# Kernel optimization log

Measured on AMD Instinct MI355X. Metric: run time of the kernel, lower is better.

Reference implementation:

```python
import jax, jax.numpy as jnp
import numpy as np

B, S, E, CS, NC, H = 4, 2048, 1024, 16, 8, 16
D = E + CS            # d_model = 1040
DH = D // H           # head_dim = 65
DFF = 4 * E           # forward_expansion * embed_size


def setup_inputs() -> dict:
    key = jax.random.key(0)
    ks = jax.random.split(key, 20)
    s = 0.02  # init scale for weights
    f32 = jnp.float32
    return {
        'x': jax.random.normal(ks[0], (B, S, E), f32),
        'conditioning': jax.random.uniform(ks[1], (B, S, CS), f32),
        # attention params (torch Linear convention: W is [out, in])
        'Wq': jax.random.normal(ks[2], (D, D), f32) * s,
        'bq': jnp.zeros((D,), f32),
        'Wv': jax.random.normal(ks[3], (D, D), f32) * s,
        'bv': jnp.zeros((D,), f32),
        'Wk': jax.random.normal(ks[4], (NC, D, D), f32) * s,  # stacked per-class key projections
        'bk': jnp.zeros((NC, D), f32),
        'Wo': jax.random.normal(ks[5], (D, D), f32) * s,
        'bo': jnp.zeros((D,), f32),
        # layernorms
        'g1': jnp.ones((E,), f32), 'bn1': jnp.zeros((E,), f32),
        'g2': jnp.ones((E,), f32), 'bn2': jnp.zeros((E,), f32),
        # feed-forward
        'Wf1': jax.random.normal(ks[6], (DFF, E), f32) * s,
        'bf1': jnp.zeros((DFF,), f32),
        'Wf2': jax.random.normal(ks[7], (E, DFF), f32) * s,
        'bf2': jnp.zeros((E,), f32),
    }


def _layernorm(x, g, b, eps=1e-5):
    m = jnp.mean(x, axis=-1, keepdims=True)
    v = jnp.mean(jnp.square(x - m), axis=-1, keepdims=True)
    return (x - m) * jax.lax.rsqrt(v + eps) * g + b


def reference(x, conditioning, Wq, bq, Wv, bv, Wk, bk, Wo, bo,
              g1, bn1, g2, bn2, Wf1, bf1, Wf2, bf2):
    # dropout is identity (eval mode)
    xn = _layernorm(x, g1, bn1)                       # [B,S,E]
    xc = jnp.concatenate([xn, conditioning], axis=-1)  # [B,S,D]

    q = (xc @ Wq.T + bq).reshape(B, S, H, DH).transpose(0, 2, 1, 3)  # [B,H,S,DH]
    v = (xc @ Wv.T + bv).reshape(B, S, H, DH).transpose(0, 2, 1, 3)

    # per-class keys: [B,C,S,D], then weighted-sum by conditioning[:,:,:NC]
    keys = jnp.einsum('bsd,cod->bcso', xc, Wk) + bk[None, :, None, :]
    w = conditioning[:, :, :NC]                        # [B,S,C]
    k = jnp.einsum('bsc,bcso->bso', w, keys)           # [B,S,D]
    k = k.reshape(B, S, H, DH).transpose(0, 2, 1, 3)   # [B,H,S,DH]

    scale = 1.0 / np.sqrt(DH).astype(np.float32)
    scores = jnp.einsum('bhqd,bhkd->bhqk', q, k) * scale
    attn = jax.nn.softmax(scores, axis=-1)
    o = jnp.einsum('bhqk,bhkd->bhqd', attn, v)
    o = o.transpose(0, 2, 1, 3).reshape(B, S, D)
    o = o @ Wo.T + bo

    h = xn + o[:, :, :E]                               # residual uses normed x
    ff = jnp.maximum(h @ Wf1.T + bf1, 0.0) @ Wf2.T + bf2
    return _layernorm(h + ff, g2, bn2)
```

## Files before the change

kernel.cpp:

```cpp
#include <hip/hip_runtime.h>
#include <hip/hip_bf16.h>
#include <math.h>

typedef __bf16 bf16;
typedef __bf16 v8bf __attribute__((ext_vector_type(8)));
typedef float v4f __attribute__((ext_vector_type(4)));

#define B_   4
#define S_   2048
#define E_   1024
#define CS_  16
#define NC_  8
#define H_   16
#define D_   1040
#define DH_  65
#define DFF_ 4096
#define M_   8192
#define KC_  1056
#define KH_  (4 * KC_)
#define KB2_ (8 * KC_)

__device__ __forceinline__ v4f mfma16(v8bf a, v8bf b, v4f c) {
    return __builtin_amdgcn_mfma_f32_16x16x32_bf16(a, b, c, 0, 0, 0);
}

__device__ __forceinline__ void async16(const bf16* g, bf16* l) {
    __builtin_amdgcn_global_load_lds(
        (const __attribute__((address_space(1))) unsigned int*)g,
        (__attribute__((address_space(3))) unsigned int*)l, 16, 0, 0);
}

__global__ __launch_bounds__(256) void k_cvt(const float* __restrict__ src,
                                             bf16* __restrict__ dst, int n) {
    int i = (blockIdx.x * 256 + threadIdx.x) * 4;
    if (i + 4 <= n) {
        float4 v = *(const float4*)(src + i);
        bf16 o[4] = {(bf16)v.x, (bf16)v.y, (bf16)v.z, (bf16)v.w};
        *(ushort4*)(dst + i) = *(const ushort4*)o;
    }
}

__global__ __launch_bounds__(256) void k_build_bk(const float* __restrict__ Wk,
                                                  bf16* __restrict__ Bp) {
    int c = blockIdx.y;
    int idx = blockIdx.x * 256 + threadIdx.x;
    if (idx >= 1040 * 130) return;
    int n = idx / 130, u = idx - n * 130;
    const float* src = Wk + ((size_t)(c * D_ + n)) * D_ + u * 8;
    float4 a = *(const float4*)src;
    float4 b = *(const float4*)(src + 4);
    bf16 o[8] = {(bf16)a.x, (bf16)a.y, (bf16)a.z, (bf16)a.w,
                 (bf16)b.x, (bf16)b.y, (bf16)b.z, (bf16)b.w};
    *(uint4*)(Bp + (size_t)n * KB2_ + c * KC_ + u * 8) = *(const uint4*)o;
}

__global__ __launch_bounds__(256) void k_scale_a(const bf16* __restrict__ xc,
                                                 const float* __restrict__ cond,
                                                 int coff, bf16* __restrict__ Ap) {
    int idx = blockIdx.x * 256 + threadIdx.x;
    int m = idx / 132, u = idx - m * 132;
    int j = u * 8;
    float4 w4 = *(const float4*)(cond + (size_t)m * CS_ + coff);
    float wv[4] = {w4.x, w4.y, w4.z, w4.w};
    bf16* dst = Ap + (size_t)m * KH_ + j;
    if (j < D_) {
        union { uint4 u4; bf16 h[8]; } src;
        src.u4 = *(const uint4*)(xc + (size_t)m * D_ + j);
        float xv[8];
#pragma unroll
        for (int e = 0; e < 8; ++e) xv[e] = (float)src.h[e];
#pragma unroll
        for (int cc = 0; cc < 4; ++cc) {
            bf16 o[8];
#pragma unroll
            for (int e = 0; e < 8; ++e) o[e] = (bf16)(xv[e] * wv[cc]);
            *(uint4*)(dst + cc * KC_) = *(const uint4*)o;
        }
    } else {
        uint4 z = {0u, 0u, 0u, 0u};
#pragma unroll
        for (int cc = 0; cc < 4; ++cc) *(uint4*)(dst + cc * KC_) = z;
    }
}

__global__ __launch_bounds__(256) void k_zero_pads(bf16* __restrict__ qp,
                                                   bf16* __restrict__ kp) {
    int i = blockIdx.x * 256 + threadIdx.x;
    int row = i >> 3, j = i & 7;
    uint4 z = {0u, 0u, 0u, 0u};
    bf16* base = (j < 4) ? qp : kp;
    ((uint4*)(base + (size_t)row * 96 + 64))[j & 3] = z;
}

__global__ __launch_bounds__(256) void k_ln_concat(
    const float* __restrict__ x, const float* __restrict__ cond,
    const float* __restrict__ g, const float* __restrict__ bn,
    bf16* __restrict__ xc)
{
    int row = blockIdx.x;
    int t = threadIdx.x;
    const float* xr = x + (size_t)row * E_;
    float4 v = *(const float4*)(xr + t * 4);
    float s = v.x + v.y + v.z + v.w;
    float ss = v.x * v.x + v.y * v.y + v.z * v.z + v.w * v.w;
#pragma unroll
    for (int off = 32; off; off >>= 1) {
        s  += __shfl_down(s, off);
        ss += __shfl_down(ss, off);
    }
    __shared__ float red[8];
    int wid = t >> 6;
    if ((t & 63) == 0) { red[wid] = s; red[4 + wid] = ss; }
    __syncthreads();
    float stot  = red[0] + red[1] + red[2] + red[3];
    float sstot = red[4] + red[5] + red[6] + red[7];
    float mean = stot * (1.0f / E_);
    float var  = sstot * (1.0f / E_) - mean * mean;
    float rs = rsqrtf(var + 1e-5f);
    bf16* xcr = xc + (size_t)row * D_;
    float vv[4] = {v.x, v.y, v.z, v.w};
#pragma unroll
    for (int j = 0; j < 4; ++j) {
        int i = t * 4 + j;
        xcr[i] = (bf16)(((vv[j] - mean) * rs) * g[i] + bn[i]);
    }
    if (t < CS_) xcr[E_ + t] = (bf16)cond[(size_t)row * CS_ + t];
}

__global__ __launch_bounds__(256) void k_gemm_k2(
    const bf16* __restrict__ A, const bf16* __restrict__ Bm,
    int koffB, bf16* __restrict__ Pout)
{
    __shared__ bf16 As[128][32];
    __shared__ bf16 Bs[128][32];
    int t = threadIdx.x;

    int pid = blockIdx.x;
    int gid = pid / 72;
    int rem = pid - gid * 72;
    int mi = gid * 8 + (rem & 7);
    int ni = rem >> 3;
    int m0 = mi << 7, n0 = ni << 7;

    int lane = t & 63, w = t >> 6;
    int wm = (w >> 1) * 64, wn = (w & 1) * 64;
    int lr = lane & 15, lq = lane >> 4;

    int row_i[2], seg_i[2];
#pragma unroll
    for (int i = 0; i < 2; ++i) { row_i[i] = (t + i * 256) >> 2; seg_i[i] = (t + i * 256) & 3; }

    v4f acc[4][4];
    v4f vzero = {0.f, 0.f, 0.f, 0.f};
#pragma unroll
    for (int mt = 0; mt < 4; ++mt)
#pragma unroll
        for (int nt = 0; nt < 4; ++nt) acc[mt][nt] = vzero;

    for (int kb = 0; kb < KH_ / 32; ++kb) {
        int k0 = kb << 5;
#pragma unroll
        for (int i = 0; i < 2; ++i) {
            async16(A + (size_t)(m0 + row_i[i]) * KH_ + k0 + seg_i[i] * 8,
                    &As[0][0] + (t + i * 256) * 8);
            async16(Bm + (size_t)(n0 + row_i[i]) * KB2_ + koffB + k0 + seg_i[i] * 8,
                    &Bs[0][0] + (t + i * 256) * 8);
        }
        __syncthreads();
        v8bf af[4], bfr[4];
#pragma unroll
        for (int mt = 0; mt < 4; ++mt) af[mt]  = *(const v8bf*)(&As[wm + mt * 16 + lr][lq * 8]);
#pragma unroll
        for (int nt = 0; nt < 4; ++nt) bfr[nt] = *(const v8bf*)(&Bs[wn + nt * 16 + lr][lq * 8]);
#pragma unroll
        for (int mt = 0; mt < 4; ++mt)
#pragma unroll
            for (int nt = 0; nt < 4; ++nt)
                acc[mt][nt] = mfma16(af[mt], bfr[nt], acc[mt][nt]);
        __syncthreads();
    }

#pragma unroll
    for (int mt = 0; mt < 4; ++mt)
#pragma unroll
        for (int reg = 0; reg < 4; ++reg) {
            int grow = m0 + wm + mt * 16 + lq * 4 + reg;
#pragma unroll
            for (int nt = 0; nt < 4; ++nt) {
                int gcol = n0 + wn + nt * 16 + lr;
                if (gcol < D_)
                    Pout[(size_t)grow * D_ + gcol] = (bf16)acc[mt][nt][reg];
            }
        }
}

__global__ __launch_bounds__(256) void k_comb_k(
    const bf16* __restrict__ P0, const bf16* __restrict__ P1,
    const float* __restrict__ condw, const float* __restrict__ bkp,
    bf16* __restrict__ kp)
{
    int idx = blockIdx.x * 256 + threadIdx.x;
    int m = idx / 1040, n = idx - m * 1040;
    float v = (float)P0[idx] + (float)P1[idx];
#pragma unroll
    for (int c = 0; c < NC_; ++c)
        v += condw[(size_t)m * CS_ + c] * bkp[(size_t)c * D_ + n];
    int h = n / 65, d = n - h * 65;
    int b = m >> 11, s = m & 2047;
    kp[(((size_t)(b * 16 + h)) * S_ + s) * 96 + d] = (bf16)v;
}

#define EP_QV  0
#define EP_O   1
#define EP_FF1 2
#define EP_FF2 3

template<int EP>
__global__ __launch_bounds__(256) void k_gemm(
    const bf16* __restrict__ A, const bf16* __restrict__ Bm,
    const float* __restrict__ bias, const float* __restrict__ bias2,
    int M, int N, int K, int lda, int ldb, int nbn,
    bf16* __restrict__ Cb, float* __restrict__ Cf, int ldc,
    const bf16* __restrict__ res, int ldres, bf16* __restrict__ Cb2)
{
    __shared__ bf16 As[128][32];
    __shared__ bf16 Bs[128][32];
    int t = threadIdx.x;

    int pid = blockIdx.x;
    int nig = 8 * nbn;
    int gid = pid / nig;
    int rem = pid - gid * nig;
    int mi = gid * 8 + (rem & 7);
    int ni = rem >> 3;
    int m0 = mi << 7, n0 = ni << 7;

    int lane = t & 63, w = t >> 6;
    int wm = (w >> 1) * 64, wn = (w & 1) * 64;
    int lr = lane & 15, lq = lane >> 4;

    int row_i[2], seg_i[2];
#pragma unroll
    for (int i = 0; i < 2; ++i) { row_i[i] = (t + i * 256) >> 2; seg_i[i] = (t + i * 256) & 3; }

    v4f acc[4][4];
    v4f vzero = {0.f, 0.f, 0.f, 0.f};
#pragma unroll
    for (int mt = 0; mt < 4; ++mt)
#pragma unroll
        for (int nt = 0; nt < 4; ++nt) acc[mt][nt] = vzero;

    const int KF = K >> 5;
    const bool KR = (K & 31) != 0;

    for (int kb = 0; kb < KF; ++kb) {
        int k0 = kb << 5;
#pragma unroll
        for (int i = 0; i < 2; ++i) {
            async16(A + (size_t)(m0 + row_i[i]) * lda + k0 + seg_i[i] * 8,
                    &As[0][0] + (t + i * 256) * 8);
            async16(Bm + (size_t)(n0 + row_i[i]) * ldb + k0 + seg_i[i] * 8,
                    &Bs[0][0] + (t + i * 256) * 8);
        }
        __syncthreads();
        v8bf af[4], bfr[4];
#pragma unroll
        for (int mt = 0; mt < 4; ++mt) af[mt]  = *(const v8bf*)(&As[wm + mt * 16 + lr][lq * 8]);
#pragma unroll
        for (int nt = 0; nt < 4; ++nt) bfr[nt] = *(const v8bf*)(&Bs[wn + nt * 16 + lr][lq * 8]);
#pragma unroll
        for (int mt = 0; mt < 4; ++mt)
#pragma unroll
            for (int nt = 0; nt < 4; ++nt)
                acc[mt][nt] = mfma16(af[mt], bfr[nt], acc[mt][nt]);
        __syncthreads();
    }
    if (KR) {
        int k0 = KF << 5;
#pragma unroll
        for (int i = 0; i < 2; ++i) {
            int gk = k0 + seg_i[i] * 8;
            uint4 val = {0u, 0u, 0u, 0u};
            if (gk + 8 <= K) val = *(const uint4*)(A + (size_t)(m0 + row_i[i]) * lda + gk);
            *(uint4*)(&As[row_i[i]][seg_i[i] * 8]) = val;
            uint4 bv = {0u, 0u, 0u, 0u};
            int gn = n0 + row_i[i];
            if (gn < N && gk + 8 <= K) bv = *(const uint4*)(Bm + (size_t)gn * ldb + gk);
            *(uint4*)(&Bs[row_i[i]][seg_i[i] * 8]) = bv;
        }
        __syncthreads();
        v8bf af[4], bfr[4];
#pragma unroll
        for (int mt = 0; mt < 4; ++mt) af[mt]  = *(const v8bf*)(&As[wm + mt * 16 + lr][lq * 8]);
#pragma unroll
        for (int nt = 0; nt < 4; ++nt) bfr[nt] = *(const v8bf*)(&Bs[wn + nt * 16 + lr][lq * 8]);
#pragma unroll
        for (int mt = 0; mt < 4; ++mt)
#pragma unroll
            for (int nt = 0; nt < 4; ++nt)
                acc[mt][nt] = mfma16(af[mt], bfr[nt], acc[mt][nt]);
        __syncthreads();
    }

#pragma unroll
    for (int mt = 0; mt < 4; ++mt) {
#pragma unroll
        for (int reg = 0; reg < 4; ++reg) {
            int grow = m0 + wm + mt * 16 + lq * 4 + reg;
#pragma unroll
            for (int nt = 0; nt < 4; ++nt) {
                int gcol = n0 + wn + nt * 16 + lr;
                float vacc = acc[mt][nt][reg];
                if constexpr (EP == EP_QV) {
                    if (gcol < D_) {
                        float o = (vacc + bias[gcol]) * 0.1789442960f;
                        int h = gcol / 65, d = gcol - h * 65;
                        int b = grow >> 11, s = grow & 2047;
                        Cb[(((size_t)(b * 16 + h)) * S_ + s) * 96 + d] = (bf16)o;
                    } else if (gcol < 2 * D_) {
                        int col = gcol - D_;
                        Cb2[(size_t)grow * D_ + col] = (bf16)(vacc + bias2[col]);
                    }
                } else if constexpr (EP == EP_O) {
                    float o = vacc + bias[gcol] + (float)res[(size_t)grow * ldres + gcol];
                    Cb[(size_t)grow * ldc + gcol] = (bf16)o;
                } else if constexpr (EP == EP_FF1) {
                    float o = vacc + bias[gcol];
                    Cb[(size_t)grow * ldc + gcol] = (bf16)fmaxf(o, 0.f);
                } else {
                    Cf[(size_t)grow * ldc + gcol] =
                        vacc + bias[gcol] + (float)res[(size_t)grow * ldres + gcol];
                }
            }
        }
    }
}

__global__ __launch_bounds__(256) void k_transpose_v(
    const bf16* __restrict__ v, bf16* __restrict__ vt)
{
    int bh = blockIdx.y, s0 = blockIdx.x * 64;
    int b = bh >> 4, h = bh & 15;
    __shared__ bf16 tile[80][65];
#pragma unroll
    for (int i = 0; i < 20; ++i) {
        int idx = threadIdx.x + i * 256;
        int d = idx % 80, sl = idx / 80;
        bf16 val = (bf16)0.f;
        if (d < DH_) val = v[((size_t)b * S_ + s0 + sl) * D_ + h * DH_ + d];
        tile[d][sl] = val;
    }
    __syncthreads();
#pragma unroll
    for (int i = 0; i < 20; ++i) {
        int idx = threadIdx.x + i * 256;
        int sl = idx % 64, d = idx / 64;
        vt[((size_t)bh * 80 + d) * S_ + s0 + sl] = tile[d][sl];
    }
}

__global__ __launch_bounds__(256) void k_attn(
    const bf16* __restrict__ qp, const bf16* __restrict__ kp,
    const bf16* __restrict__ vt, bf16* __restrict__ o)
{
    int bh = blockIdx.y;
    int s0 = blockIdx.x * 64;
    int b = bh >> 4, h = bh & 15;
    int t = threadIdx.x, lane = t & 63, w = t >> 6;
    int lr = lane & 15, lq = lane >> 4;

    __shared__ bf16 Ks[64][104];
    __shared__ bf16 Vs[80][72];
    __shared__ bf16 QP[64 * 104];

    const bf16* qbase = qp + ((size_t)bh * S_ + s0) * 96;
#pragma unroll
    for (int i = 0; i < 3; ++i) {
        int idx = t + i * 256;
        int row = idx / 12, seg = idx % 12;
        *(uint4*)(&QP[row * 104 + seg * 8]) = *(const uint4*)(qbase + (size_t)row * 96 + seg * 8);
    }
    __syncthreads();
    v8bf qreg[3];
#pragma unroll
    for (int ks = 0; ks < 3; ++ks)
        qreg[ks] = *(const v8bf*)(&QP[(w * 16 + lr) * 104 + ks * 32 + lq * 8]);
    __syncthreads();

    bf16* Ps = &QP[w * (16 * 72)];

    float m_r[4], l_r[4];
    v4f o_acc[5];
    v4f vzero = {0.f, 0.f, 0.f, 0.f};
#pragma unroll
    for (int r = 0; r < 4; ++r) { m_r[r] = -1e30f; l_r[r] = 0.f; }
#pragma unroll
    for (int nt = 0; nt < 5; ++nt) o_acc[nt] = vzero;

    for (int kb = 0; kb < S_ / 64; ++kb) {
        const bf16* kbase = kp + ((size_t)bh * S_ + kb * 64) * 96;
#pragma unroll
        for (int i = 0; i < 3; ++i) {
            int idx = t + i * 256;
            int row = idx / 12, seg = idx % 12;
            *(uint4*)(&Ks[row][seg * 8]) = *(const uint4*)(kbase + (size_t)row * 96 + seg * 8);
        }
#pragma unroll
        for (int i = 0; i < 3; ++i) {
            int idx = t + i * 256;
            if (idx < 640) {
                int d = idx >> 3, seg = idx & 7;
                *(uint4*)(&Vs[d][seg * 8]) =
                    *(const uint4*)(vt + ((size_t)bh * 80 + d) * S_ + kb * 64 + seg * 8);
            }
        }
        __syncthreads();

        v4f sacc[4];
#pragma unroll
        for (int nt = 0; nt < 4; ++nt) sacc[nt] = vzero;
#pragma unroll
        for (int ks = 0; ks < 3; ++ks) {
#pragma unroll
            for (int nt = 0; nt < 4; ++nt) {
                v8bf bk2 = *(const v8bf*)(&Ks[nt * 16 + lr][ks * 32 + lq * 8]);
                sacc[nt] = mfma16(qreg[ks], bk2, sacc[nt]);
            }
        }

        float alpha[4];
#pragma unroll
        for (int r = 0; r < 4; ++r) {
            float mx = fmaxf(fmaxf(sacc[0][r], sacc[1][r]), fmaxf(sacc[2][r], sacc[3][r]));
#pragma unroll
            for (int off = 1; off < 16; off <<= 1) mx = fmaxf(mx, __shfl_xor(mx, off));
            float mnew = fmaxf(m_r[r], mx);
            alpha[r] = __builtin_amdgcn_exp2f(m_r[r] - mnew);
            float ps = 0.f;
#pragma unroll
            for (int nt = 0; nt < 4; ++nt) {
                float p = __builtin_amdgcn_exp2f(sacc[nt][r] - mnew);
                sacc[nt][r] = p;
                ps += p;
            }
#pragma unroll
            for (int off = 1; off < 16; off <<= 1) ps += __shfl_xor(ps, off);
            l_r[r] = l_r[r] * alpha[r] + ps;
            m_r[r] = mnew;
        }

#pragma unroll
        for (int nt = 0; nt < 4; ++nt)
#pragma unroll
            for (int r = 0; r < 4; ++r)
                Ps[(lq * 4 + r) * 72 + nt * 16 + lr] = (bf16)sacc[nt][r];
        asm volatile("s_waitcnt lgkmcnt(0)" ::: "memory");

#pragma unroll
        for (int nt = 0; nt < 5; ++nt)
#pragma unroll
            for (int r = 0; r < 4; ++r) o_acc[nt][r] *= alpha[r];

#pragma unroll
        for (int kt = 0; kt < 2; ++kt) {
            v8bf ap = *(const v8bf*)(&Ps[lr * 72 + kt * 32 + lq * 8]);
#pragma unroll
            for (int nt = 0; nt < 5; ++nt) {
                v8bf bv2 = *(const v8bf*)(&Vs[nt * 16 + lr][kt * 32 + lq * 8]);
                o_acc[nt] = mfma16(ap, bv2, o_acc[nt]);
            }
        }
        __syncthreads();
    }

    float inv[4];
#pragma unroll
    for (int r = 0; r < 4; ++r) inv[r] = 1.0f / l_r[r];
    int token = b * S_ + s0 + w * 16 + lq * 4;
#pragma unroll
    for (int nt = 0; nt < 5; ++nt) {
        int d = nt * 16 + lr;
        if (d < DH_) {
#pragma unroll
            for (int r = 0; r < 4; ++r)
                o[(size_t)(token + r) * D_ + h * DH_ + d] = (bf16)(o_acc[nt][r] * inv[r]);
        }
    }
}

__global__ __launch_bounds__(256) void k_ln_out(
    const float* __restrict__ z, const float* __restrict__ g,
    const float* __restrict__ bn, float* __restrict__ out)
{
    int row = blockIdx.x;
    int t = threadIdx.x;
    const float* zr = z + (size_t)row * E_;
    float4 v = *(const float4*)(zr + t * 4);
    float s = v.x + v.y + v.z + v.w;
    float ss = v.x * v.x + v.y * v.y + v.z * v.z + v.w * v.w;
#pragma unroll
    for (int off = 32; off; off >>= 1) {
        s  += __shfl_down(s, off);
        ss += __shfl_down(ss, off);
    }
    __shared__ float red[8];
    int wid = t >> 6;
    if ((t & 63) == 0) { red[wid] = s; red[4 + wid] = ss; }
    __syncthreads();
    float stot  = red[0] + red[1] + red[2] + red[3];
    float sstot = red[4] + red[5] + red[6] + red[7];
    float mean = stot * (1.0f / E_);
    float var  = sstot * (1.0f / E_) - mean * mean;
    float rs = rsqrtf(var + 1e-5f);
    float* outr = out + (size_t)row * E_;
    float vv[4] = {v.x, v.y, v.z, v.w};
#pragma unroll
    for (int j = 0; j < 4; ++j) {
        int i = t * 4 + j;
        outr[i] = ((vv[j] - mean) * rs) * g[i] + bn[i];
    }
}

extern "C" void kernel_launch(void* const* d_in, const int* in_sizes, int n_in,
                              void* d_out, int out_size, void* d_ws, size_t ws_size,
                              hipStream_t stream) {
    const float* x    = (const float*)d_in[0];
    const float* cond = (const float*)d_in[1];
    const float* Wq   = (const float*)d_in[2];
    const float* bq   = (const float*)d_in[3];
    const float* Wv   = (const float*)d_in[4];
    const float* bv   = (const float*)d_in[5];
    const float* Wk   = (const float*)d_in[6];
    const float* bk   = (const float*)d_in[7];
    const float* Wo   = (const float*)d_in[8];
    const float* bo   = (const float*)d_in[9];
    const float* g1   = (const float*)d_in[10];
    const float* bn1  = (const float*)d_in[11];
    const float* g2   = (const float*)d_in[12];
    const float* bn2  = (const float*)d_in[13];
    const float* Wf1  = (const float*)d_in[14];
    const float* bf1  = (const float*)d_in[15];
    const float* Wf2  = (const float*)d_in[16];
    const float* bf2  = (const float*)d_in[17];
    float* out = (float*)d_out;

    char* ws = (char*)d_ws;
    bf16* Wqv_b = (bf16*)(ws + 0);
    bf16* Wo_b  = (bf16*)(ws + 4526080);
    bf16* Wf1_b = (bf16*)(ws + 6656000);
    bf16* Wf2_b = (bf16*)(ws + 15044608);
    bf16*  xc   = (bf16*)(ws + 23433216);
    bf16*  Bpk  = (bf16*)(ws + 40472576);
    bf16*  Apk  = (bf16*)(ws + 59936768);
    bf16*  P0k  = (bf16*)(ws + 129142784);
    bf16*  P1k  = (bf16*)(ws + 146182144);
    bf16*  qp   = (bf16*)(ws + 40472576);
    bf16*  kp   = (bf16*)(ws + 65638400);
    bf16*  vb   = (bf16*)(ws + 90804224);
    bf16*  hb   = (bf16*)(ws + 90804224);
    bf16*  vtb  = (bf16*)(ws + 107843584);
    bf16*  ob   = (bf16*)(ws + 128815104);
    bf16*  ff1  = (bf16*)(ws + 23433216);
    float* zb   = (float*)(ws + 107843584);

    k_cvt<<<(1081600 / 4 + 255) / 256, 256, 0, stream>>>(Wq, Wqv_b, 1081600);
    k_cvt<<<(1081600 / 4 + 255) / 256, 256, 0, stream>>>(Wv, Wqv_b + 1081600, 1081600);
    k_cvt<<<(1064960 / 4 + 255) / 256, 256, 0, stream>>>(Wo, Wo_b, 1064960);
    k_cvt<<<(4194304 / 4 + 255) / 256, 256, 0, stream>>>(Wf1, Wf1_b, 4194304);
    k_cvt<<<(4194304 / 4 + 255) / 256, 256, 0, stream>>>(Wf2, Wf2_b, 4194304);

    k_ln_concat<<<M_, 256, 0, stream>>>(x, cond, g1, bn1, xc);

    k_build_bk<<<dim3((1040 * 130 + 255) / 256, 8), 256, 0, stream>>>(Wk, Bpk);
    k_scale_a<<<(M_ * 132) / 256, 256, 0, stream>>>(xc, cond, 0, Apk);
    k_gemm_k2<<<576, 256, 0, stream>>>(Apk, Bpk, 0, P0k);
    k_scale_a<<<(M_ * 132) / 256, 256, 0, stream>>>(xc, cond, 4, Apk);
    k_gemm_k2<<<576, 256, 0, stream>>>(Apk, Bpk, KH_, P1k);

    k_zero_pads<<<4096, 256, 0, stream>>>(qp, kp);
    k_comb_k<<<(M_ * D_) / 256, 256, 0, stream>>>(P0k, P1k, cond, bk, kp);

    k_gemm<EP_QV><<<64 * 17, 256, 0, stream>>>(xc, Wqv_b, bq, bv, M_, 2 * D_, D_, D_, D_, 17,
                                               qp, nullptr, 0, nullptr, 0, vb);

    k_transpose_v<<<dim3(S_ / 64, 64), 256, 0, stream>>>(vb, vtb);
    k_attn<<<dim3(S_ / 64, 64), 256, 0, stream>>>(qp, kp, vtb, ob);

    k_gemm<EP_O><<<64 * 8, 256, 0, stream>>>(ob, Wo_b, bo, nullptr, M_, E_, D_, D_, D_, 8,
                                             hb, nullptr, E_, xc, D_, nullptr);
    k_gemm<EP_FF1><<<64 * 32, 256, 0, stream>>>(hb, Wf1_b, bf1, nullptr, M_, DFF_, E_, E_, E_, 32,
                                                ff1, nullptr, DFF_, nullptr, 0, nullptr);
    k_gemm<EP_FF2><<<64 * 8, 256, 0, stream>>>(ff1, Wf2_b, bf2, nullptr, M_, E_, DFF_, DFF_, DFF_, 8,
                                               nullptr, zb, E_, hb, E_, nullptr);

    k_ln_out<<<M_, 256, 0, stream>>>(zb, g2, bn2, out);
}
```

Before: 1.068 ms.

## Prefetch K/V tiles into registers and transpose MFMA operands in attention

The attention kernel now loads the next K and V tiles into registers while the current tile is being computed, overlapping global loads with MFMA work. It swaps the MFMA operand order so each lane holds a single query row. That cuts the softmax row reductions to two cross-lane shuffles instead of four per row, and lets P be written to LDS with packed stores. It also loads Q directly from global memory without staging it through LDS, adds s_setprio around the MFMA blocks, and sets a launch bound of 4 blocks per CU. The register prefetch raises register pressure, which could limit occupancy or cause spills.

```diff
diff --git a/kernel.cpp b/kernel.cpp
--- a/kernel.cpp
+++ b/kernel.cpp
@@ -359,7 +359,7 @@
     }
 }
 
-__global__ __launch_bounds__(256) void k_attn(
+__global__ __launch_bounds__(256, 4) void k_attn(
     const bf16* __restrict__ qp, const bf16* __restrict__ kp,
     const bf16* __restrict__ vt, bf16* __restrict__ o)
 {
@@ -371,121 +371,128 @@
 
     __shared__ bf16 Ks[64][104];
     __shared__ bf16 Vs[80][72];
-    __shared__ bf16 QP[64 * 104];
-
-    const bf16* qbase = qp + ((size_t)bh * S_ + s0) * 96;
+    __shared__ bf16 Psh[4][16 * 72];
+    bf16* Ps = Psh[w];
+
+    const bf16* qbase = qp + ((size_t)bh * S_ + s0 + w * 16 + lr) * 96;
+    v8bf qreg[3];
+#pragma unroll
+    for (int ks = 0; ks < 3; ++ks)
+        qreg[ks] = *(const v8bf*)(qbase + ks * 32 + lq * 8);
+
+    int kro[3], kso[3], vdi[3], vsi[3];
+    bool vld[3];
 #pragma unroll
     for (int i = 0; i < 3; ++i) {
         int idx = t + i * 256;
-        int row = idx / 12, seg = idx % 12;
-        *(uint4*)(&QP[row * 104 + seg * 8]) = *(const uint4*)(qbase + (size_t)row * 96 + seg * 8);
-    }
-    __syncthreads();
-    v8bf qreg[3];
-#pragma unroll
-    for (int ks = 0; ks < 3; ++ks)
-        qreg[ks] = *(const v8bf*)(&QP[(w * 16 + lr) * 104 + ks * 32 + lq * 8]);
-    __syncthreads();
-
-    bf16* Ps = &QP[w * (16 * 72)];
-
-    float m_r[4], l_r[4];
+        kro[i] = idx / 12; kso[i] = idx % 12;
+        vld[i] = idx < 640; vdi[i] = idx >> 3; vsi[i] = idx & 7;
+    }
+
+    const bf16* kpb = kp + (size_t)bh * S_ * 96;
+    const bf16* vpb = vt + (size_t)bh * 80 * S_;
+
+    uint4 krg[3], vrg[3];
+#pragma unroll
+    for (int i = 0; i < 3; ++i)
+        krg[i] = *(const uint4*)(kpb + (size_t)kro[i] * 96 + kso[i] * 8);
+#pragma unroll
+    for (int i = 0; i < 3; ++i)
+        if (vld[i]) vrg[i] = *(const uint4*)(vpb + (size_t)vdi[i] * S_ + vsi[i] * 8);
+
+    float m_s = -1e30f, l_s = 0.f;
     v4f o_acc[5];
     v4f vzero = {0.f, 0.f, 0.f, 0.f};
 #pragma unroll
-    for (int r = 0; r < 4; ++r) { m_r[r] = -1e30f; l_r[r] = 0.f; }
-#pragma unroll
     for (int nt = 0; nt < 5; ++nt) o_acc[nt] = vzero;
 
     for (int kb = 0; kb < S_ / 64; ++kb) {
-        const bf16* kbase = kp + ((size_t)bh * S_ + kb * 64) * 96;
-#pragma unroll
-        for (int i = 0; i < 3; ++i) {
-            int idx = t + i * 256;
-            int row = idx / 12, seg = idx % 12;
-            *(uint4*)(&Ks[row][seg * 8]) = *(const uint4*)(kbase + (size_t)row * 96 + seg * 8);
-        }
-#pragma unroll
-        for (int i = 0; i < 3; ++i) {
-            int idx = t + i * 256;
-            if (idx < 640) {
-                int d = idx >> 3, seg = idx & 7;
-                *(uint4*)(&Vs[d][seg * 8]) =
-                    *(const uint4*)(vt + ((size_t)bh * 80 + d) * S_ + kb * 64 + seg * 8);
+#pragma unroll
+        for (int i = 0; i < 3; ++i)
+            *(uint4*)(&Ks[kro[i]][kso[i] * 8]) = krg[i];
+#pragma unroll
+        for (int i = 0; i < 3; ++i)
+            if (vld[i]) *(uint4*)(&Vs[vdi[i]][vsi[i] * 8]) = vrg[i];
+        __syncthreads();
+
+        if (kb + 1 < S_ / 64) {
+            const bf16* kn = kpb + (size_t)(kb + 1) * (64 * 96);
+#pragma unroll
+            for (int i = 0; i < 3; ++i)
+                krg[i] = *(const uint4*)(kn + (size_t)kro[i] * 96 + kso[i] * 8);
+#pragma unroll
+            for (int i = 0; i < 3; ++i)
+                if (vld[i]) vrg[i] = *(const uint4*)(vpb + (size_t)vdi[i] * S_ + (kb + 1) * 64 + vsi[i] * 8);
+        }
+
+        v4f sacc[4];
+#pragma unroll
+        for (int kt = 0; kt < 4; ++kt) sacc[kt] = vzero;
+        __builtin_amdgcn_s_setprio(1);
+#pragma unroll
+        for (int ks = 0; ks < 3; ++ks)
+#pragma unroll
+            for (int kt = 0; kt < 4; ++kt) {
+                v8bf kf = *(const v8bf*)(&Ks[kt * 16 + lr][ks * 32 + lq * 8]);
+                sacc[kt] = mfma16(kf, qreg[ks], sacc[kt]);
             }
-        }
-        __syncthreads();
-
-        v4f sacc[4];
-#pragma unroll
-        for (int nt = 0; nt < 4; ++nt) sacc[nt] = vzero;
-#pragma unroll
-        for (int ks = 0; ks < 3; ++ks) {
-#pragma unroll
-            for (int nt = 0; nt < 4; ++nt) {
-                v8bf bk2 = *(const v8bf*)(&Ks[nt * 16 + lr][ks * 32 + lq * 8]);
-                sacc[nt] = mfma16(qreg[ks], bk2, sacc[nt]);
+        __builtin_amdgcn_s_setprio(0);
+
+        float mx = sacc[0][0];
+#pragma unroll
+        for (int kt = 0; kt < 4; ++kt)
+#pragma unroll
+            for (int r = 0; r < 4; ++r) mx = fmaxf(mx, sacc[kt][r]);
+        mx = fmaxf(mx, __shfl_xor(mx, 16));
+        mx = fmaxf(mx, __shfl_xor(mx, 32));
+        float mnew = fmaxf(m_s, mx);
+        float alpha = __builtin_amdgcn_exp2f(m_s - mnew);
+        float ps = 0.f;
+#pragma unroll
+        for (int kt = 0; kt < 4; ++kt) {
+            bf16 p4[4];
+#pragma unroll
+            for (int r = 0; r < 4; ++r) {
+                float p = __builtin_amdgcn_exp2f(sacc[kt][r] - mnew);
+                ps += p;
+                p4[r] = (bf16)p;
             }
-        }
-
-        float alpha[4];
-#pragma unroll
-        for (int r = 0; r < 4; ++r) {
-            float mx = fmaxf(fmaxf(sacc[0][r], sacc[1][r]), fmaxf(sacc[2][r], sacc[3][r]));
-#pragma unroll
-            for (int off = 1; off < 16; off <<= 1) mx = fmaxf(mx, __shfl_xor(mx, off));
-            float mnew = fmaxf(m_r[r], mx);
-            alpha[r] = __builtin_amdgcn_exp2f(m_r[r] - mnew);
-            float ps = 0.f;
-#pragma unroll
-            for (int nt = 0; nt < 4; ++nt) {
-                float p = __builtin_amdgcn_exp2f(sacc[nt][r] - mnew);
-                sacc[nt][r] = p;
-                ps += p;
+            *(uint2*)(&Ps[lr * 72 + kt * 16 + lq * 4]) = *(const uint2*)p4;
+        }
+        ps += __shfl_xor(ps, 16);
+        ps += __shfl_xor(ps, 32);
+        l_s = l_s * alpha + ps;
+        m_s = mnew;
+
+#pragma unroll
+        for (int nt = 0; nt < 5; ++nt)
+#pragma unroll
+            for (int r = 0; r < 4; ++r) o_acc[nt][r] *= alpha;
+
+        asm volatile("s_waitcnt lgkmcnt(0)" ::: "memory");
+
+        __builtin_amdgcn_s_setprio(1);
+#pragma unroll
+        for (int kt = 0; kt < 2; ++kt) {
+            v8bf pf = *(const v8bf*)(&Ps[lr * 72 + kt * 32 + lq * 8]);
+#pragma unroll
+            for (int nt = 0; nt < 5; ++nt) {
+                v8bf vf = *(const v8bf*)(&Vs[nt * 16 + lr][kt * 32 + lq * 8]);
+                o_acc[nt] = mfma16(vf, pf, o_acc[nt]);
             }
-#pragma unroll
-            for (int off = 1; off < 16; off <<= 1) ps += __shfl_xor(ps, off);
-            l_r[r] = l_r[r] * alpha[r] + ps;
-            m_r[r] = mnew;
-        }
-
-#pragma unroll
-        for (int nt = 0; nt < 4; ++nt)
-#pragma unroll
-            for (int r = 0; r < 4; ++r)
-                Ps[(lq * 4 + r) * 72 + nt * 16 + lr] = (bf16)sacc[nt][r];
-        asm volatile("s_waitcnt lgkmcnt(0)" ::: "memory");
-
-#pragma unroll
-        for (int nt = 0; nt < 5; ++nt)
-#pragma unroll
-            for (int r = 0; r < 4; ++r) o_acc[nt][r] *= alpha[r];
-
-#pragma unroll
-        for (int kt = 0; kt < 2; ++kt) {
-            v8bf ap = *(const v8bf*)(&Ps[lr * 72 + kt * 32 + lq * 8]);
-#pragma unroll
-            for (int nt = 0; nt < 5; ++nt) {
-                v8bf bv2 = *(const v8bf*)(&Vs[nt * 16 + lr][kt * 32 + lq * 8]);
-                o_acc[nt] = mfma16(ap, bv2, o_acc[nt]);
-            }
-        }
-        __syncthreads();
-    }
-
-    float inv[4];
-#pragma unroll
-    for (int r = 0; r < 4; ++r) inv[r] = 1.0f / l_r[r];
-    int token = b * S_ + s0 + w * 16 + lq * 4;
-#pragma unroll
-    for (int nt = 0; nt < 5; ++nt) {
-        int d = nt * 16 + lr;
-        if (d < DH_) {
-#pragma unroll
-            for (int r = 0; r < 4; ++r)
-                o[(size_t)(token + r) * D_ + h * DH_ + d] = (bf16)(o_acc[nt][r] * inv[r]);
-        }
-    }
+        }
+        __builtin_amdgcn_s_setprio(0);
+        __syncthreads();
+    }
+
+    float inv = 1.0f / l_s;
+    bf16* obase = o + (size_t)(b * S_ + s0 + w * 16 + lr) * D_ + h * DH_;
+#pragma unroll
+    for (int nt = 0; nt < 4; ++nt)
+#pragma unroll
+        for (int r = 0; r < 4; ++r)
+            obase[nt * 16 + lq * 4 + r] = (bf16)(o_acc[nt][r] * inv);
+    if (lq == 0) obase[64] = (bf16)(o_acc[4][0] * inv);
 }
 
 __global__ __launch_bounds__(256) void k_ln_out(
```

Measured after the change: 1.208 ms. 13.1% more time.
